# Optimization experiments

Measured on AMD Instinct MI355X. Metric: run time of the kernel, lower is better.

Reference implementation:

```python
import jax, jax.numpy as jnp
import numpy as np

B = 8192          # batch size (positions)
FPP = 32          # active features per position (NNUE: 32 pieces)
NNZ = B * FPP     # 262144
FT_OUT = 1024
N_FEAT = 49152
N_VFEAT = 768


def setup_inputs() -> dict:
    key = jax.random.key(0)
    ks = jax.random.split(key, 6)
    stm_feat = jax.random.randint(ks[0], (NNZ,), 0, N_FEAT, dtype=jnp.int32)
    nstm_feat = jax.random.randint(ks[1], (NNZ,), 0, N_FEAT, dtype=jnp.int32)
    batch_idx = jnp.repeat(jnp.arange(B, dtype=jnp.int32), FPP)  # exactly FPP feats per sample
    values = jnp.ones((NNZ,), jnp.float32)
    s = 0.02
    W_ft = jax.random.normal(ks[2], (N_FEAT, FT_OUT), jnp.float32) * s   # Linear weight, pre-transposed [in, out]
    b_ft = jax.random.normal(ks[3], (FT_OUT,), jnp.float32) * s
    W_fft = jax.random.normal(ks[4], (N_VFEAT, FT_OUT), jnp.float32) * s
    b_fft = jnp.zeros((FT_OUT,), jnp.float32)
    W_out = jax.random.normal(ks[5], (2 * FT_OUT, 1), jnp.float32) * s
    b_out = jnp.zeros((1,), jnp.float32)
    return {
        "values": values, "stm_feat": stm_feat, "nstm_feat": nstm_feat,
        "batch_idx": batch_idx, "W_ft": W_ft, "b_ft": b_ft,
        "W_fft": W_fft, "b_fft": b_fft, "W_out": W_out, "b_out": b_out,
        "size": B,
    }


def reference(values, stm_feat, nstm_feat, batch_idx, W_ft, b_ft, W_fft, b_fft, W_out, b_out, size):
    # sparse @ W.T + b  ==  per-sample gather-sum of weight rows (embedding-bag) + bias
    def side_ft(feat):
        vw = values[:, None]                                   # [nnz,1]
        g = jax.ops.segment_sum(W_ft[feat] * vw, batch_idx, num_segments=size)        # [B, FT_OUT]
        gv = jax.ops.segment_sum(W_fft[feat % N_VFEAT] * vw, batch_idx, num_segments=size)
        return g + gv + b_ft + b_fft

    stm_ft = side_ft(stm_feat)
    nstm_ft = side_ft(nstm_feat)
    hidden = jnp.clip(jnp.concatenate([stm_ft, nstm_ft], axis=1), 0.0, 1.0)  # [B, 2*FT_OUT]
    return jax.nn.sigmoid(hidden @ W_out + b_out)                            # [B, 1]
```

## Files before the change

### kernel.cpp

```cpp
#include <hip/hip_runtime.h>

#define BATCH   8192
#define FPP     32
#define FT_OUT  1024
#define N_VFEAT 768
#define N_FEAT  49152

#define WQ_BYTES   ((size_t)N_FEAT * FT_OUT)
#define WS_NEEDED  (WQ_BYTES + (size_t)N_FEAT * 4)

typedef signed char c8 __attribute__((ext_vector_type(8)));

__global__ __launch_bounds__(256) void build_combined_i8(
    const float* __restrict__ W_ft,
    const float* __restrict__ W_fft,
    signed char* __restrict__ Wq,
    float*       __restrict__ scales)
{
    const int f = blockIdx.x;
    const int t = threadIdx.x;

    const float4 a = *reinterpret_cast<const float4*>(W_ft  + (size_t)f * FT_OUT + 4 * t);
    const float4 g = *reinterpret_cast<const float4*>(W_fft + (size_t)(f % N_VFEAT) * FT_OUT + 4 * t);
    const float c0 = a.x + g.x, c1 = a.y + g.y, c2 = a.z + g.z, c3 = a.w + g.w;

    float m = fmaxf(fmaxf(fabsf(c0), fabsf(c1)), fmaxf(fabsf(c2), fabsf(c3)));
#pragma unroll
    for (int o = 32; o > 0; o >>= 1)
        m = fmaxf(m, __shfl_down(m, o, 64));

    __shared__ float s_m[4];
    if ((t & 63) == 0) s_m[t >> 6] = m;
    __syncthreads();
    const float am  = fmaxf(fmaxf(fmaxf(s_m[0], s_m[1]), fmaxf(s_m[2], s_m[3])), 1e-20f);
    const float inv = 127.0f / am;
    if (t == 0) scales[f] = am / 127.0f;

    int q0 = (int)rintf(c0 * inv);
    int q1 = (int)rintf(c1 * inv);
    int q2 = (int)rintf(c2 * inv);
    int q3 = (int)rintf(c3 * inv);
    q0 = max(-127, min(127, q0));
    q1 = max(-127, min(127, q1));
    q2 = max(-127, min(127, q2));
    q3 = max(-127, min(127, q3));
    char4 pk;
    pk.x = (signed char)q0; pk.y = (signed char)q1;
    pk.z = (signed char)q2; pk.w = (signed char)q3;
    *reinterpret_cast<char4*>(Wq + (size_t)f * FT_OUT + 4 * t) = pk;
}

__global__ __launch_bounds__(256) void nnue_fwd_i8(
    const float*       __restrict__ values,
    const int*         __restrict__ stm_feat,
    const int*         __restrict__ nstm_feat,
    const signed char* __restrict__ Wq,
    const float*       __restrict__ scales,
    const float*       __restrict__ b_ft,
    const float*       __restrict__ b_fft,
    const float*       __restrict__ W_out,
    const float*       __restrict__ b_out,
    float*             __restrict__ out)
{
    const int b    = blockIdx.x;
    const int tid  = threadIdx.x;
    const int side = tid >> 7;
    const int lane = tid & 127;
    const int c0   = lane * 8;

    __shared__ int   s_off[2][FPP];
    __shared__ float s_vs [2][FPP];
    __shared__ float s_red[4];

    if (tid < 64) {
        const int sd = tid >> 5;
        const int k  = tid & 31;
        const int f  = (sd ? nstm_feat : stm_feat)[b * FPP + k];
        s_off[sd][k] = f * FT_OUT;
        s_vs [sd][k] = values[b * FPP + k] * scales[f];
    }
    __syncthreads();

    float acc[8];
#pragma unroll
    for (int j = 0; j < 8; ++j) acc[j] = 0.0f;

#pragma unroll 4
    for (int k = 0; k < FPP; ++k) {
        const c8 q = *reinterpret_cast<const c8*>(Wq + s_off[side][k] + c0);
        const float vs = s_vs[side][k];
#pragma unroll
        for (int j = 0; j < 8; ++j)
            acc[j] += vs * (float)q[j];
    }

    float partial = 0.0f;
#pragma unroll
    for (int j = 0; j < 8; ++j) {
        float h = acc[j] + b_ft[c0 + j] + b_fft[c0 + j];
        h = fminf(fmaxf(h, 0.0f), 1.0f);
        partial += h * W_out[side * FT_OUT + c0 + j];
    }

#pragma unroll
    for (int o = 32; o > 0; o >>= 1)
        partial += __shfl_down(partial, o, 64);

    const int wv = tid >> 6;
    if ((tid & 63) == 0) s_red[wv] = partial;
    __syncthreads();

    if (tid == 0) {
        float x = s_red[0] + s_red[1] + s_red[2] + s_red[3] + b_out[0];
        out[b] = 1.0f / (1.0f + __expf(-x));
    }
}

__global__ __launch_bounds__(256) void nnue_fwd_f32(
    const float* __restrict__ values,
    const int*   __restrict__ stm_feat,
    const int*   __restrict__ nstm_feat,
    const float* __restrict__ W_ft,
    const float* __restrict__ b_ft,
    const float* __restrict__ W_fft,
    const float* __restrict__ b_fft,
    const float* __restrict__ W_out,
    const float* __restrict__ b_out,
    float*       __restrict__ out)
{
    const int b    = blockIdx.x;
    const int tid  = threadIdx.x;
    const int side = tid >> 7;
    const int lane = tid & 127;
    const int c0   = lane * 8;

    __shared__ int   s_off_ft [2][FPP];
    __shared__ int   s_off_fft[2][FPP];
    __shared__ float s_val[FPP];
    __shared__ float s_red[4];

    if (tid < FPP) {
        int f = stm_feat[b * FPP + tid];
        s_off_ft [0][tid] = f * FT_OUT;
        s_off_fft[0][tid] = (f % N_VFEAT) * FT_OUT;
        s_val[tid] = values[b * FPP + tid];
    } else if (tid < 2 * FPP) {
        int k = tid - FPP;
        int f = nstm_feat[b * FPP + k];
        s_off_ft [1][k] = f * FT_OUT;
        s_off_fft[1][k] = (f % N_VFEAT) * FT_OUT;
    }
    __syncthreads();

    float acc[8];
#pragma unroll
    for (int j = 0; j < 8; ++j) acc[j] = 0.0f;

#pragma unroll 4
    for (int k = 0; k < FPP; ++k) {
        const float* ra = W_ft  + s_off_ft [side][k] + c0;
        const float* rg = W_fft + s_off_fft[side][k] + c0;
        const float4 a0 = *reinterpret_cast<const float4*>(ra);
        const float4 a1 = *reinterpret_cast<const float4*>(ra + 4);
        const float4 g0 = *reinterpret_cast<const float4*>(rg);
        const float4 g1 = *reinterpret_cast<const float4*>(rg + 4);
        const float v = s_val[k];
        acc[0] += (a0.x + g0.x) * v;  acc[1] += (a0.y + g0.y) * v;
        acc[2] += (a0.z + g0.z) * v;  acc[3] += (a0.w + g0.w) * v;
        acc[4] += (a1.x + g1.x) * v;  acc[5] += (a1.y + g1.y) * v;
        acc[6] += (a1.z + g1.z) * v;  acc[7] += (a1.w + g1.w) * v;
    }

    float partial = 0.0f;
#pragma unroll
    for (int j = 0; j < 8; ++j) {
        float h = acc[j] + b_ft[c0 + j] + b_fft[c0 + j];
        h = fminf(fmaxf(h, 0.0f), 1.0f);
        partial += h * W_out[side * FT_OUT + c0 + j];
    }
#pragma unroll
    for (int o = 32; o > 0; o >>= 1)
        partial += __shfl_down(partial, o, 64);
    const int wv = tid >> 6;
    if ((tid & 63) == 0) s_red[wv] = partial;
    __syncthreads();
    if (tid == 0) {
        float x = s_red[0] + s_red[1] + s_red[2] + s_red[3] + b_out[0];
        out[b] = 1.0f / (1.0f + __expf(-x));
    }
}

extern "C" void kernel_launch(void* const* d_in, const int* in_sizes, int n_in,
                              void* d_out, int out_size, void* d_ws, size_t ws_size,
                              hipStream_t stream) {
    const float* values    = (const float*)d_in[0];
    const int*   stm_feat  = (const int*)d_in[1];
    const int*   nstm_feat = (const int*)d_in[2];
    const float* W_ft      = (const float*)d_in[4];
    const float* b_ft      = (const float*)d_in[5];
    const float* W_fft     = (const float*)d_in[6];
    const float* b_fft     = (const float*)d_in[7];
    const float* W_out     = (const float*)d_in[8];
    const float* b_out     = (const float*)d_in[9];
    float*       out       = (float*)d_out;

    if (ws_size >= WS_NEEDED) {
        signed char* Wq     = (signed char*)d_ws;
        float*       scales = (float*)((char*)d_ws + WQ_BYTES);

        build_combined_i8<<<N_FEAT, 256, 0, stream>>>(W_ft, W_fft, Wq, scales);

        nnue_fwd_i8<<<BATCH, 256, 0, stream>>>(
            values, stm_feat, nstm_feat, Wq, scales, b_ft, b_fft, W_out, b_out, out);
    } else {
        nnue_fwd_f32<<<BATCH, 256, 0, stream>>>(
            values, stm_feat, nstm_feat, W_ft, b_ft, W_fft, b_fft, W_out, b_out, out);
    }
}
```

Measured before the change: 359.0 us.

## Use one wavefront per row in int8 build and two samples per block in forward

The quantize kernel now gives each feature row to a single wavefront, so the max reduction needs only xor shuffles and no shared memory or block barrier. It also uses nontemporal loads for the large W_ft stream. The forward kernel handles two samples per block, with one wavefront per sample-side, 16 int8 columns per lane and vectorized bias/output-weight loads. The aim is fewer blocks and barriers and wider memory accesses, at the cost of more registers per thread.

Measured after the change: 359.1 us. No clear change (+0.0%).

```diff
diff --git a/kernel.cpp b/kernel.cpp
--- a/kernel.cpp
+++ b/kernel.cpp
@@ -9,7 +9,8 @@
 #define WQ_BYTES   ((size_t)N_FEAT * FT_OUT)
 #define WS_NEEDED  (WQ_BYTES + (size_t)N_FEAT * 4)
 
-typedef signed char c8 __attribute__((ext_vector_type(8)));
+typedef signed char c16 __attribute__((ext_vector_type(16)));
+typedef float       f4  __attribute__((ext_vector_type(4)));
 
 __global__ __launch_bounds__(256) void build_combined_i8(
     const float* __restrict__ W_ft,
@@ -17,37 +18,52 @@
     signed char* __restrict__ Wq,
     float*       __restrict__ scales)
 {
-    const int f = blockIdx.x;
-    const int t = threadIdx.x;
-
-    const float4 a = *reinterpret_cast<const float4*>(W_ft  + (size_t)f * FT_OUT + 4 * t);
-    const float4 g = *reinterpret_cast<const float4*>(W_fft + (size_t)(f % N_VFEAT) * FT_OUT + 4 * t);
-    const float c0 = a.x + g.x, c1 = a.y + g.y, c2 = a.z + g.z, c3 = a.w + g.w;
-
-    float m = fmaxf(fmaxf(fabsf(c0), fabsf(c1)), fmaxf(fabsf(c2), fabsf(c3)));
+    const int wave = threadIdx.x >> 6;
+    const int lane = threadIdx.x & 63;
+    const int f    = blockIdx.x * 4 + wave;
+    const int fm   = (blockIdx.x % (N_VFEAT / 4)) * 4 + wave;
+
+    const float* a = W_ft  + (size_t)f  * FT_OUT;
+    const float* g = W_fft + (size_t)fm * FT_OUT;
+
+    float c[16];
+#pragma unroll
+    for (int ch = 0; ch < 4; ++ch) {
+        const f4 av = __builtin_nontemporal_load(
+            reinterpret_cast<const f4*>(a + ch * 256 + lane * 4));
+        const f4 gv = *reinterpret_cast<const f4*>(g + ch * 256 + lane * 4);
+        c[ch * 4 + 0] = av.x + gv.x;
+        c[ch * 4 + 1] = av.y + gv.y;
+        c[ch * 4 + 2] = av.z + gv.z;
+        c[ch * 4 + 3] = av.w + gv.w;
+    }
+
+    float m = 0.0f;
+#pragma unroll
+    for (int j = 0; j < 16; ++j) m = fmaxf(m, fabsf(c[j]));
 #pragma unroll
     for (int o = 32; o > 0; o >>= 1)
-        m = fmaxf(m, __shfl_down(m, o, 64));
-
-    __shared__ float s_m[4];
-    if ((t & 63) == 0) s_m[t >> 6] = m;
-    __syncthreads();
-    const float am  = fmaxf(fmaxf(fmaxf(s_m[0], s_m[1]), fmaxf(s_m[2], s_m[3])), 1e-20f);
+        m = fmaxf(m, __shfl_xor(m, o, 64));
+
+    const float am  = fmaxf(m, 1e-20f);
     const float inv = 127.0f / am;
-    if (t == 0) scales[f] = am / 127.0f;
-
-    int q0 = (int)rintf(c0 * inv);
-    int q1 = (int)rintf(c1 * inv);
-    int q2 = (int)rintf(c2 * inv);
-    int q3 = (int)rintf(c3 * inv);
-    q0 = max(-127, min(127, q0));
-    q1 = max(-127, min(127, q1));
-    q2 = max(-127, min(127, q2));
-    q3 = max(-127, min(127, q3));
-    char4 pk;
-    pk.x = (signed char)q0; pk.y = (signed char)q1;
-    pk.z = (signed char)q2; pk.w = (signed char)q3;
-    *reinterpret_cast<char4*>(Wq + (size_t)f * FT_OUT + 4 * t) = pk;
+    if (lane == 0) scales[f] = am / 127.0f;
+
+#pragma unroll
+    for (int ch = 0; ch < 4; ++ch) {
+        int q0 = (int)rintf(c[ch * 4 + 0] * inv);
+        int q1 = (int)rintf(c[ch * 4 + 1] * inv);
+        int q2 = (int)rintf(c[ch * 4 + 2] * inv);
+        int q3 = (int)rintf(c[ch * 4 + 3] * inv);
+        q0 = max(-127, min(127, q0));
+        q1 = max(-127, min(127, q1));
+        q2 = max(-127, min(127, q2));
+        q3 = max(-127, min(127, q3));
+        char4 pk;
+        pk.x = (signed char)q0; pk.y = (signed char)q1;
+        pk.z = (signed char)q2; pk.w = (signed char)q3;
+        *reinterpret_cast<char4*>(Wq + (size_t)f * FT_OUT + ch * 256 + lane * 4) = pk;
+    }
 }
 
 __global__ __launch_bounds__(256) void nnue_fwd_i8(
@@ -62,57 +78,64 @@
     const float*       __restrict__ b_out,
     float*             __restrict__ out)
 {
-    const int b    = blockIdx.x;
     const int tid  = threadIdx.x;
-    const int side = tid >> 7;
-    const int lane = tid & 127;
-    const int c0   = lane * 8;
-
-    __shared__ int   s_off[2][FPP];
-    __shared__ float s_vs [2][FPP];
-    __shared__ float s_red[4];
-
-    if (tid < 64) {
-        const int sd = tid >> 5;
+    const int wave = tid >> 6;
+    const int lane = tid & 63;
+    const int bl   = wave >> 1;
+    const int sd   = wave & 1;
+    const int c0   = lane * 16;
+
+    __shared__ int   s_off[2][2][FPP];
+    __shared__ float s_vs [2][2][FPP];
+    __shared__ float s_red[2][2];
+
+    if (tid < 128) {
+        const int lb = tid >> 6;
+        const int ls = (tid >> 5) & 1;
         const int k  = tid & 31;
-        const int f  = (sd ? nstm_feat : stm_feat)[b * FPP + k];
-        s_off[sd][k] = f * FT_OUT;
-        s_vs [sd][k] = values[b * FPP + k] * scales[f];
-    }
-    __syncthreads();
-
-    float acc[8];
-#pragma unroll
-    for (int j = 0; j < 8; ++j) acc[j] = 0.0f;
-
-#pragma unroll 4
+        const int b  = blockIdx.x * 2 + lb;
+        const int f  = (ls ? nstm_feat : stm_feat)[b * FPP + k];
+        s_off[lb][ls][k] = f * FT_OUT;
+        s_vs [lb][ls][k] = values[b * FPP + k] * scales[f];
+    }
+    __syncthreads();
+
+    float acc[16];
+#pragma unroll
+    for (int j = 0; j < 16; ++j) acc[j] = 0.0f;
+
+#pragma unroll 8
     for (int k = 0; k < FPP; ++k) {
-        const c8 q = *reinterpret_cast<const c8*>(Wq + s_off[side][k] + c0);
-        const float vs = s_vs[side][k];
-#pragma unroll
-        for (int j = 0; j < 8; ++j)
+        const c16 q = *reinterpret_cast<const c16*>(Wq + s_off[bl][sd][k] + c0);
+        const float vs = s_vs[bl][sd][k];
+#pragma unroll
+        for (int j = 0; j < 16; ++j)
             acc[j] += vs * (float)q[j];
     }
 
     float partial = 0.0f;
 #pragma unroll
-    for (int j = 0; j < 8; ++j) {
-        float h = acc[j] + b_ft[c0 + j] + b_fft[c0 + j];
-        h = fminf(fmaxf(h, 0.0f), 1.0f);
-        partial += h * W_out[side * FT_OUT + c0 + j];
+    for (int ch = 0; ch < 4; ++ch) {
+        const float4 bf = *reinterpret_cast<const float4*>(b_ft  + c0 + 4 * ch);
+        const float4 bg = *reinterpret_cast<const float4*>(b_fft + c0 + 4 * ch);
+        const float4 wo = *reinterpret_cast<const float4*>(W_out + sd * FT_OUT + c0 + 4 * ch);
+        float h;
+        h = acc[ch * 4 + 0] + bf.x + bg.x; h = fminf(fmaxf(h, 0.0f), 1.0f); partial += h * wo.x;
+        h = acc[ch * 4 + 1] + bf.y + bg.y; h = fminf(fmaxf(h, 0.0f), 1.0f); partial += h * wo.y;
+        h = acc[ch * 4 + 2] + bf.z + bg.z; h = fminf(fmaxf(h, 0.0f), 1.0f); partial += h * wo.z;
+        h = acc[ch * 4 + 3] + bf.w + bg.w; h = fminf(fmaxf(h, 0.0f), 1.0f); partial += h * wo.w;
     }
 
 #pragma unroll
     for (int o = 32; o > 0; o >>= 1)
         partial += __shfl_down(partial, o, 64);
 
-    const int wv = tid >> 6;
-    if ((tid & 63) == 0) s_red[wv] = partial;
-    __syncthreads();
-
-    if (tid == 0) {
-        float x = s_red[0] + s_red[1] + s_red[2] + s_red[3] + b_out[0];
-        out[b] = 1.0f / (1.0f + __expf(-x));
+    if (lane == 0) s_red[bl][sd] = partial;
+    __syncthreads();
+
+    if (tid < 2) {
+        float x = s_red[tid][0] + s_red[tid][1] + b_out[0];
+        out[blockIdx.x * 2 + tid] = 1.0f / (1.0f + __expf(-x));
     }
 }
 
@@ -208,9 +231,9 @@
         signed char* Wq     = (signed char*)d_ws;
         float*       scales = (float*)((char*)d_ws + WQ_BYTES);
 
-        build_combined_i8<<<N_FEAT, 256, 0, stream>>>(W_ft, W_fft, Wq, scales);
-
-        nnue_fwd_i8<<<BATCH, 256, 0, stream>>>(
+        build_combined_i8<<<N_FEAT / 4, 256, 0, stream>>>(W_ft, W_fft, Wq, scales);
+
+        nnue_fwd_i8<<<BATCH / 2, 256, 0, stream>>>(
             values, stm_feat, nstm_feat, Wq, scales, b_ft, b_fft, W_out, b_out, out);
     } else {
         nnue_fwd_f32<<<BATCH, 256, 0, stream>>>(
```
